# Kernel optimization log

Hardware: AMD Instinct MI355X
Metric: run time of the kernel (lower is better)

The kernel has to match this reference:

```python
import jax, jax.numpy as jnp
import numpy as np

N_ENTITIES = 4096
FEATURE_DIM = 512
CELLS = 39
PAIRS = 8192


def setup_inputs() -> dict:
    key = jax.random.key(0)
    k_emb, k_idx, k_wg, k_wl = jax.random.split(key, 4)
    embedding = jax.random.normal(k_emb, (N_ENTITIES, FEATURE_DIM), dtype=jnp.float32)
    index = jax.random.randint(k_idx, (CELLS, PAIRS, 2), 0, N_ENTITIES, dtype=jnp.int32)
    # kaiming_uniform-style scale for the global bilinear weight
    bound_g = np.sqrt(6.0 / FEATURE_DIM)
    weights_global = jax.random.uniform(k_wg, (FEATURE_DIM, FEATURE_DIM), minval=-bound_g, maxval=bound_g, dtype=jnp.float32)
    # per-cell diagonal scaling vectors (original stores them as [d,1] params)
    weights_local = jax.random.uniform(k_wl, (CELLS, FEATURE_DIM), minval=-bound_g, maxval=bound_g, dtype=jnp.float32)
    return {"embedding": embedding, "index": index,
            "weights_global": weights_global, "weights_local": weights_local}


def reference(embedding, index, weights_global, weights_local):
    # Original per-cell math: einsum('bn,nm,mj,jk,bk->b', A, diag(wl), W, diag(wl), B)
    # diag(wl) @ ... is just elementwise scaling of the gathered embeddings, so:
    #   out[c,p] = sum_{n,k} (A[c,p,n]*wl[c,n]) * W[n,k] * (B[c,p,k]*wl[c,k])
    wl = weights_local[:, None, :]                      # [C,1,d]
    A = embedding[index[..., 0]] * wl                   # [C,P,d]
    B = embedding[index[..., 1]] * wl                   # [C,P,d]
    return jnp.einsum('cpn,nk,cpk->cp', A, weights_global, B)  # [C,P]
```

## Files before the change

### kernel.cpp

```cpp
#include <hip/hip_runtime.h>
#include <stdint.h>

#define NE 4096
#define FD 512
#define NCELLS 39
#define NPAIRS 8192
#define NT (FD / 64)

typedef __attribute__((ext_vector_type(8))) short short8;
typedef __attribute__((ext_vector_type(8))) unsigned short ushort8;
typedef __attribute__((ext_vector_type(4))) float f32x4;
typedef __attribute__((ext_vector_type(4))) unsigned int uint4v;

__device__ __forceinline__ unsigned short f2bf(float f) {
  union { float f; uint32_t u; } v; v.f = f;
  uint32_t u = v.u;
  return (unsigned short)((u + 0x7fffu + ((u >> 16) & 1u)) >> 16);
}
__device__ __forceinline__ float bf2f(unsigned short b) {
  return __uint_as_float(((uint32_t)b) << 16);
}

__device__ __forceinline__ void async16(const void* g, void* l) {
  __builtin_amdgcn_global_load_lds((const __attribute__((address_space(1))) void*)g,
                                   (__attribute__((address_space(3))) void*)l, 16, 0, 0);
}

__global__ __launch_bounds__(256) void conv_e(const float* __restrict__ E,
                                              unsigned short* __restrict__ Ebf) {
  const int i = blockIdx.x * 256 + threadIdx.x;
  const float4 v = ((const float4*)E)[i];
  ushort4 o;
  o.x = f2bf(v.x); o.y = f2bf(v.y); o.z = f2bf(v.z); o.w = f2bf(v.w);
  ((ushort4*)Ebf)[i] = o;
}

__global__ __launch_bounds__(256) void prep_w(const float* __restrict__ W,
                                              const float* __restrict__ wl,
                                              unsigned short* __restrict__ Wt,
                                              int c0) {
  __shared__ float tile[32][33];
  const int ci = blockIdx.z;
  const int tn = blockIdx.x * 32, tk = blockIdx.y * 32;
  const int tx = threadIdx.x & 31, ty = threadIdx.x >> 5;
  const float* wlr = wl + (size_t)(c0 + ci) * FD;
#pragma unroll
  for (int i = 0; i < 4; i++) {
    int n = tn + ty + i * 8;
    tile[ty + i * 8][tx] = W[(size_t)n * FD + tk + tx] * wlr[n];
  }
  __syncthreads();
  unsigned short* dst = Wt + (size_t)ci * FD * FD;
#pragma unroll
  for (int i = 0; i < 4; i++) {
    int kout = tk + ty + i * 8;
    dst[(size_t)kout * FD + tn + tx] = f2bf(tile[tx][ty + i * 8] * wlr[kout]);
  }
}

__global__ __launch_bounds__(512, 2) void gemm_k(const unsigned short* __restrict__ Ebf,
                                                 const unsigned short* __restrict__ Wt,
                                                 unsigned short* __restrict__ U) {
  __shared__ unsigned short lds[2][2][2][128 * 64];
  const int t = threadIdx.x;
  const int id = blockIdx.x;
  int bx, by, ci;
  if (gridDim.x == 32 * NCELLS) {
    if (id < 1024) {
      const int a = id & 7, m = (id >> 3) & 7, h = (id >> 6) & 3, w = id >> 8;
      bx = m | ((a & 1) << 3);
      const int cb = (w << 4) | ((a >> 1) << 2) | h;
      ci = cb >> 1; by = cb & 1;
    } else {
      const int r = id - 1024;
      bx = r & 15;
      const int cb = 64 + (r >> 4);
      ci = cb >> 1; by = cb & 1;
    }
  } else {
    const int xcd = id & 7;
    const int j = id >> 3;
    bx = xcd * 2 + (j & 1);
    by = (j >> 1) & 1;
    ci = j >> 2;
  }

  const unsigned short* Ag = Ebf + (size_t)bx * 256 * FD;
  const unsigned short* Bg = Wt + (size_t)ci * FD * FD + (size_t)by * 256 * FD;

  const int wave = t >> 6, lane = t & 63;
  const int wm = wave >> 2, wn = wave & 3;
  const int lr = lane & 15, lq = lane >> 4;

  const int pg0 = t, pg1 = 512 + t;
  const int sr0 = pg0 >> 3, sg0 = pg0 & 7;
  const int sr1 = pg1 >> 3, sg1 = pg1 & 7;
  const int soff0 = sr0 * FD + ((sg0 ^ (sr0 & 7)) << 3);
  const int soff1 = sr1 * FD + ((sg1 ^ (sr1 & 7)) << 3);
  const int loff0 = pg0 * 8, loff1 = pg1 * 8;

  const int swz0 = (lq ^ (lr & 7)) << 3;
  const int swz1 = ((4 + lq) ^ (lr & 7)) << 3;

#define STAGE(OP, HALF, KT, GBASE)                                                \
  do {                                                                            \
    const int bi_ = (KT) & 1;                       \
    const int kt_ = (KT) < NT ? (KT) : (NT - 1);       \
    const unsigned short* gb_ = (GBASE) + (size_t)(HALF) * (128 * FD) + kt_ * 64; \
    unsigned short* d_ = &lds[bi_][OP][HALF][0];                                  \
    async16(gb_ + soff0, d_ + loff0);                                             \
    async16(gb_ + soff1, d_ + loff1);                                             \
  } while (0)

  short8 a[8], b01[4], b23[4];
  f32x4 acc[8][4];
#pragma unroll
  for (int i = 0; i < 8; i++)
#pragma unroll
    for (int j2 = 0; j2 < 4; j2++) acc[i][j2] = (f32x4){0.f, 0.f, 0.f, 0.f};

#define LDA(BUF, MSET)                                                  \
  do {                                                                  \
    const unsigned short* p_ = &lds[BUF][0][wm][0];                     \
    _Pragma("unroll") for (int mi_ = 0; mi_ < 4; ++mi_) {               \
      const int row_ = (MSET) * 64 + mi_ * 16 + lr;                     \
      a[mi_ * 2 + 0] = *(const short8*)&p_[row_ * 64 + swz0];           \
      a[mi_ * 2 + 1] = *(const short8*)&p_[row_ * 64 + swz1];           \
    }                                                                   \
  } while (0)

#define LDB(BUF, NSET, DST)                                             \
  do {                                                                  \
    const unsigned short* p_ = &lds[BUF][1][wn >> 1][0];                \
    _Pragma("unroll") for (int ni_ = 0; ni_ < 2; ++ni_) {               \
      const int row_ = (wn & 1) * 64 + ((NSET) * 2 + ni_) * 16 + lr;    \
      (DST)[ni_ * 2 + 0] = *(const short8*)&p_[row_ * 64 + swz0];       \
      (DST)[ni_ * 2 + 1] = *(const short8*)&p_[row_ * 64 + swz1];       \
    }                                                                   \
  } while (0)

#define MMA(MSET, NSET, B)                                                               \
  do {                                                                                   \
    __builtin_amdgcn_s_setprio(1);                                                       \
    _Pragma("unroll") for (int mi_ = 0; mi_ < 4; ++mi_)                                  \
    _Pragma("unroll") for (int ni_ = 0; ni_ < 2; ++ni_)                                  \
    _Pragma("unroll") for (int s_ = 0; s_ < 2; ++s_)                                     \
      acc[(MSET) * 4 + mi_][(NSET) * 2 + ni_] = __builtin_amdgcn_mfma_f32_16x16x32_bf16( \
          a[mi_ * 2 + s_], (B)[ni_ * 2 + s_],                                            \
          acc[(MSET) * 4 + mi_][(NSET) * 2 + ni_], 0, 0, 0);                             \
    __builtin_amdgcn_s_setprio(0);                                                       \
  } while (0)

#define SYNC_LG()                                        \
  do {                                                   \
    __builtin_amdgcn_s_barrier();                        \
    asm volatile("s_waitcnt lgkmcnt(0)" ::: "memory");   \
  } while (0)

  STAGE(1, 0, 0, Bg); STAGE(0, 0, 0, Ag); STAGE(1, 1, 0, Bg); STAGE(0, 1, 0, Ag);
  STAGE(1, 0, 1, Bg); STAGE(0, 0, 1, Ag);
  asm volatile("s_waitcnt vmcnt(4)" ::: "memory");
  __builtin_amdgcn_s_barrier();

  for (int it = 0; it < NT / 2; ++it) {
    const int k1 = 2 * it + 1, k2 = 2 * it + 2, k3 = 2 * it + 3;
    LDA(0, 0); LDB(0, 0, b01);
    STAGE(1, 1, k1, Bg);
    SYNC_LG(); MMA(0, 0, b01); __builtin_amdgcn_s_barrier();
    LDB(0, 1, b23);
    STAGE(0, 1, k1, Ag);
    SYNC_LG(); MMA(0, 1, b23); __builtin_amdgcn_s_barrier();
    LDA(0, 1);
    STAGE(1, 0, k2, Bg);
    SYNC_LG(); MMA(1, 1, b23); __builtin_amdgcn_s_barrier();
    STAGE(0, 0, k2, Ag);
    __builtin_amdgcn_s_barrier();
    MMA(1, 0, b01);
    asm volatile("s_waitcnt vmcnt(4)" ::: "memory");
    __builtin_amdgcn_s_barrier();
    LDA(1, 0); LDB(1, 0, b01);
    STAGE(1, 1, k2, Bg);
    SYNC_LG(); MMA(0, 0, b01); __builtin_amdgcn_s_barrier();
    LDB(1, 1, b23);
    STAGE(0, 1, k2, Ag);
    SYNC_LG(); MMA(0, 1, b23); __builtin_amdgcn_s_barrier();
    LDA(1, 1);
    STAGE(1, 0, k3, Bg);
    SYNC_LG(); MMA(1, 1, b23); __builtin_amdgcn_s_barrier();
    STAGE(0, 0, k3, Ag);
    __builtin_amdgcn_s_barrier();
    MMA(1, 0, b01);
    asm volatile("s_waitcnt vmcnt(4)" ::: "memory");
    __builtin_amdgcn_s_barrier();
  }

  unsigned short* Up = U + (size_t)ci * NE * FD;
  const int mrow0 = bx * 256 + wm * 128;
  const int ncol0 = by * 256 + wn * 64;
#pragma unroll
  for (int mi = 0; mi < 8; ++mi) {
    const int mbase = mrow0 + mi * 16 + lq * 4;
#pragma unroll
    for (int ni = 0; ni < 4; ++ni) {
      const int n = ncol0 + ni * 16 + lr;
#pragma unroll
      for (int r = 0; r < 4; ++r)
        Up[(size_t)(mbase + r) * FD + n] = f2bf(acc[mi][ni][r]);
    }
  }
#undef STAGE
#undef LDA
#undef LDB
#undef MMA
#undef SYNC_LG
}

__global__ __launch_bounds__(256) void dot_k(const unsigned short* __restrict__ U,
                                             const unsigned short* __restrict__ Ebf,
                                             const int* __restrict__ index,
                                             float* __restrict__ out,
                                             int c0) {
  const int ci = blockIdx.y;
  const int c = c0 + ci;
  const int wave = threadIdx.x >> 6, lane = threadIdx.x & 63;
  const unsigned short* Uc = U + (size_t)ci * NE * FD;
  const size_t cp = (size_t)c * NPAIRS;
  const int2* idx2 = (const int2*)index + cp;
  float* op = out + cp;
  const int pbase = (blockIdx.x * 4 + wave) * 32;

  const int b1 = lane & 1, b2 = (lane >> 1) & 1, b4 = (lane >> 2) & 1;

  for (int batch = 0; batch < 4; batch++) {
    const int pb = pbase + batch * 8;
    int2 id[8];
#pragma unroll
    for (int b = 0; b < 8; b++) id[b] = idx2[pb + b];
    uint4v uv[8], ev[8];
#pragma unroll
    for (int b = 0; b < 8; b++) {
      uv[b] = *(const uint4v*)(Uc + (size_t)id[b].x * FD + lane * 8);
      ev[b] = *(const uint4v*)(Ebf + (size_t)id[b].y * FD + lane * 8);
    }
    float v[8];
#pragma unroll
    for (int b = 0; b < 8; b++) {
      const ushort8 u = *(const ushort8*)&uv[b];
      const ushort8 e = *(const ushort8*)&ev[b];
      float s = 0.f;
#pragma unroll
      for (int q = 0; q < 8; q++) s += bf2f(u[q]) * bf2f(e[q]);
      v[b] = s;
    }
    float w[4];
#pragma unroll
    for (int q = 0; q < 4; q++) {
      const float keep = b1 ? v[2 * q + 1] : v[2 * q];
      const float send = b1 ? v[2 * q] : v[2 * q + 1];
      w[q] = keep + __shfl_xor(send, 1, 64);
    }
    float u2[2];
#pragma unroll
    for (int q = 0; q < 2; q++) {
      const float keep = b2 ? w[2 * q + 1] : w[2 * q];
      const float send = b2 ? w[2 * q] : w[2 * q + 1];
      u2[q] = keep + __shfl_xor(send, 2, 64);
    }
    float f;
    {
      const float keep = b4 ? u2[1] : u2[0];
      const float send = b4 ? u2[0] : u2[1];
      f = keep + __shfl_xor(send, 4, 64);
    }
    f += __shfl_xor(f, 8, 64);
    f += __shfl_xor(f, 16, 64);
    f += __shfl_xor(f, 32, 64);
    if (lane < 8) op[pb + lane] = f;
  }
}

__global__ __launch_bounds__(256) void naive_k(const float* __restrict__ emb,
                                               const int* __restrict__ index,
                                               const float* __restrict__ W,
                                               const float* __restrict__ wl,
                                               float* __restrict__ out) {
  __shared__ float bs[FD];
  __shared__ float red[256];
  const int c = blockIdx.y, p = blockIdx.x;
  const int i0 = index[((size_t)c * NPAIRS + p) * 2];
  const int i1 = index[((size_t)c * NPAIRS + p) * 2 + 1];
  const float* wlc = wl + (size_t)c * FD;
  for (int k = threadIdx.x; k < FD; k += 256) bs[k] = emb[(size_t)i1 * FD + k] * wlc[k];
  __syncthreads();
  float s = 0.f;
  for (int n = threadIdx.x; n < FD; n += 256) {
    const float* wr = W + (size_t)n * FD;
    float tacc = 0.f;
    for (int k = 0; k < FD; k++) tacc += wr[k] * bs[k];
    s += tacc * emb[(size_t)i0 * FD + n] * wlc[n];
  }
  red[threadIdx.x] = s;
  __syncthreads();
  for (int st = 128; st > 0; st >>= 1) {
    if (threadIdx.x < st) red[threadIdx.x] += red[threadIdx.x + st];
    __syncthreads();
  }
  if (threadIdx.x == 0) out[(size_t)c * NPAIRS + p] = red[0];
}

extern "C" void kernel_launch(void* const* d_in, const int* in_sizes, int n_in,
                              void* d_out, int out_size, void* d_ws, size_t ws_size,
                              hipStream_t stream) {
  const float* emb = (const float*)d_in[0];
  const int* index = (const int*)d_in[1];
  const float* Wg = (const float*)d_in[2];
  const float* wl = (const float*)d_in[3];
  float* out = (float*)d_out;

  const size_t ebytes = (size_t)NE * FD * 2;
  const size_t wtcell = (size_t)FD * FD * 2;
  const size_t ucell = (size_t)NE * FD * 2;
  size_t avail = ws_size > ebytes ? ws_size - ebytes : 0;
  int G = (int)(avail / (wtcell + ucell));
  if (G > NCELLS) G = NCELLS;

  if (G < 1) {
    naive_k<<<dim3(NPAIRS, NCELLS), 256, 0, stream>>>(emb, index, Wg, wl, out);
    return;
  }

  unsigned short* Ebf = (unsigned short*)d_ws;
  unsigned short* Wt = (unsigned short*)((char*)d_ws + ebytes);
  unsigned short* U = (unsigned short*)((char*)d_ws + ebytes + (size_t)G * wtcell);

  conv_e<<<dim3((NE * FD / 4) / 256), 256, 0, stream>>>(emb, Ebf);
  for (int c0 = 0; c0 < NCELLS; c0 += G) {
    int g = (NCELLS - c0 < G) ? (NCELLS - c0) : G;
    prep_w<<<dim3(FD / 32, FD / 32, g), 256, 0, stream>>>(Wg, wl, Wt, c0);
    gemm_k<<<dim3(32 * g), 512, 0, stream>>>(Ebf, Wt, U);
    dot_k<<<dim3(NPAIRS / 128, g), 256, 0, stream>>>(U, Ebf, index, out, c0);
  }
}
```

Measured before the change: 240.4 us.

## Fuse embedding/weight prep into one kernel and stage GEMM epilogue through LDS

Merges the embedding bf16 conversion and the per-cell weight scaling/transpose into a single init kernel when the whole workspace fits all cells, which cuts the launch count. The GEMM epilogue now writes the accumulators into swizzled LDS and then stores 16-byte row-contiguous chunks to global memory, replacing scattered 2-byte stores. This adds an extra LDS round trip and barriers at the end of the GEMM.

```diff
diff --git a/kernel.cpp b/kernel.cpp
--- a/kernel.cpp
+++ b/kernel.cpp
@@ -24,6 +24,41 @@
 __device__ __forceinline__ void async16(const void* g, void* l) {
   __builtin_amdgcn_global_load_lds((const __attribute__((address_space(1))) void*)g,
                                    (__attribute__((address_space(3))) void*)l, 16, 0, 0);
+}
+
+__global__ __launch_bounds__(256) void init_k(const float* __restrict__ E,
+                                              unsigned short* __restrict__ Ebf,
+                                              const float* __restrict__ W,
+                                              const float* __restrict__ wl,
+                                              unsigned short* __restrict__ Wt) {
+  __shared__ float tile[32][33];
+  const int bid = blockIdx.x;
+  if (bid < 2048) {
+    const int i = bid * 256 + threadIdx.x;
+    const float4 v = ((const float4*)E)[i];
+    ushort4 o;
+    o.x = f2bf(v.x); o.y = f2bf(v.y); o.z = f2bf(v.z); o.w = f2bf(v.w);
+    ((ushort4*)Ebf)[i] = o;
+    return;
+  }
+  const int pid = bid - 2048;
+  const int ci = pid >> 8;
+  const int rem = pid & 255;
+  const int tn = (rem & 15) * 32, tk = (rem >> 4) * 32;
+  const int tx = threadIdx.x & 31, ty = threadIdx.x >> 5;
+  const float* wlr = wl + (size_t)ci * FD;
+#pragma unroll
+  for (int i = 0; i < 4; i++) {
+    int n = tn + ty + i * 8;
+    tile[ty + i * 8][tx] = W[(size_t)n * FD + tk + tx] * wlr[n];
+  }
+  __syncthreads();
+  unsigned short* dst = Wt + (size_t)ci * FD * FD;
+#pragma unroll
+  for (int i = 0; i < 4; i++) {
+    int kout = tk + ty + i * 8;
+    dst[(size_t)kout * FD + tn + tx] = f2bf(tile[tx][ty + i * 8] * wlr[kout]);
+  }
 }
 
 __global__ __launch_bounds__(256) void conv_e(const float* __restrict__ E,
@@ -194,18 +229,30 @@
     __builtin_amdgcn_s_barrier();
   }
 
-  unsigned short* Up = U + (size_t)ci * NE * FD;
-  const int mrow0 = bx * 256 + wm * 128;
-  const int ncol0 = by * 256 + wn * 64;
-#pragma unroll
-  for (int mi = 0; mi < 8; ++mi) {
-    const int mbase = mrow0 + mi * 16 + lq * 4;
-#pragma unroll
-    for (int ni = 0; ni < 4; ++ni) {
-      const int n = ncol0 + ni * 16 + lr;
-#pragma unroll
-      for (int r = 0; r < 4; ++r)
-        Up[(size_t)(mbase + r) * FD + n] = f2bf(acc[mi][ni][r]);
+  asm volatile("s_waitcnt vmcnt(0)" ::: "memory");
+  __syncthreads();
+  {
+    unsigned short* Ut = &lds[0][0][0][0];
+    const int mrow0w = wm * 128, ncol0w = wn * 64;
+#pragma unroll
+    for (int mi = 0; mi < 8; ++mi)
+#pragma unroll
+      for (int ni = 0; ni < 4; ++ni)
+#pragma unroll
+        for (int r = 0; r < 4; ++r) {
+          const int row = mrow0w + mi * 16 + lq * 4 + r;
+          const int col = ncol0w + ni * 16 + lr;
+          Ut[row * 256 + (col ^ ((row & 12) << 2))] = f2bf(acc[mi][ni][r]);
+        }
+    __syncthreads();
+    unsigned short* Up = U + (size_t)ci * NE * FD + (size_t)(bx * 256) * FD + by * 256;
+    const int lrow = t >> 5;
+    const int le = (t & 31) * 8;
+#pragma unroll
+    for (int pass = 0; pass < 16; ++pass) {
+      const int row = pass * 16 + lrow;
+      const ushort8 vv = *(const ushort8*)&Ut[row * 256 + (le ^ ((row & 12) << 2))];
+      *(ushort8*)&Up[(size_t)row * FD + le] = vv;
     }
   }
 #undef STAGE
@@ -333,6 +380,13 @@
   unsigned short* Wt = (unsigned short*)((char*)d_ws + ebytes);
   unsigned short* U = (unsigned short*)((char*)d_ws + ebytes + (size_t)G * wtcell);
 
+  if (G >= NCELLS) {
+    init_k<<<dim3(2048 + NCELLS * 256), 256, 0, stream>>>(emb, Ebf, Wg, wl, Wt);
+    gemm_k<<<dim3(32 * NCELLS), 512, 0, stream>>>(Ebf, Wt, U);
+    dot_k<<<dim3(NPAIRS / 128, NCELLS), 256, 0, stream>>>(U, Ebf, index, out, 0);
+    return;
+  }
+
   conv_e<<<dim3((NE * FD / 4) / 256), 256, 0, stream>>>(emb, Ebf);
   for (int c0 = 0; c0 < NCELLS; c0 += G) {
     int g = (NCELLS - c0 < G) ? (NCELLS - c0) : G;
```

New measurement: 239.9 us. No clear change (-0.2%).
